# Optimization experiments

Measured on AMD Instinct MI355X. Metric: run time of the kernel, lower is better.

## Reference

```python
import jax, jax.numpy as jnp
import numpy as np

TAU = 0.07
EPS = 1e-6  # torch CosineSimilarity eps


def setup_inputs() -> dict:
    key = jax.random.key(0)
    k1, k2, k3 = jax.random.split(key, 3)
    n, d, n_classes = 8192, 256, 1024
    imitation_embeds = jax.random.normal(k1, (n, d), dtype=jnp.float32)
    recording_embeds = jax.random.normal(k2, (n, d), dtype=jnp.float32)
    labels = jax.random.randint(k3, (n,), 0, n_classes, dtype=jnp.int64)
    return {
        "imitation_embeds": imitation_embeds,
        "recording_embeds": recording_embeds,
        "labels": labels,
    }


def reference(imitation_embeds, recording_embeds, labels):
    n = imitation_embeds.shape[0]
    # cosine similarity with per-vector norm clamp (torch semantics)
    im_n = imitation_embeds / jnp.maximum(
        jnp.linalg.norm(imitation_embeds, axis=1, keepdims=True), EPS)
    rec_n = recording_embeds / jnp.maximum(
        jnp.linalg.norm(recording_embeds, axis=1, keepdims=True), EPS)
    i2r = jnp.einsum("nd,md->nm", im_n, rec_n) / TAU  # [n, n]

    same = labels[:, None] == labels[None, :]          # [n, n] bool
    eye = jnp.eye(n, dtype=bool)
    # original: mask = ~(same ^ diag_embed(diag(same))); diag(same) is all True
    # -> keep the diagonal (positive) and all different-label negatives
    mask = ~(same ^ eye)

    # per-row masked log-softmax evaluated at the diagonal entry:
    # log_softmax(row[mask])[pos_of_diag] = i2r[i,i] - logsumexp(row over mask)
    lse = jax.nn.logsumexp(jnp.where(mask, i2r, -jnp.inf), axis=1)  # [n]
    loss = -jnp.mean(jnp.diagonal(i2r) - lse)
    return loss
```

## Files before the change

kernel.cpp:

```cpp
#include <hip/hip_runtime.h>

#define N 8192
#define D 256
#define INV_TAU 14.285714285714286f
#define LOG2E 1.4426950408889634f
#define EPSN 1e-6f

#define RT 128
#define CT 64
#define CSPLIT 16
#define CPB (N / CSPLIT)
#define NTILES (CPB / CT)
#define MAXC 96

typedef unsigned int u32x4 __attribute__((ext_vector_type(4)));
typedef __bf16 bf16x8 __attribute__((ext_vector_type(8)));
typedef float f32x4 __attribute__((ext_vector_type(4)));

__device__ inline unsigned short f2bf(float x) {
    unsigned int u = __builtin_bit_cast(unsigned int, x);
    u += 0x7fffu + ((u >> 16) & 1u);
    return (unsigned short)(u >> 16);
}

__device__ inline float bf2f(unsigned short u) {
    return __builtin_bit_cast(float, (unsigned int)u << 16);
}

__global__ void ntx_prep(const float* __restrict__ im, const float* __restrict__ rec,
                         unsigned short* __restrict__ A, unsigned short* __restrict__ Bm,
                         float* __restrict__ diag, float* __restrict__ rowsum,
                         int* __restrict__ cnt, float* __restrict__ out) {
    const int wave = threadIdx.x >> 6;
    const int lane = threadIdx.x & 63;
    const int row  = blockIdx.x * 4 + wave;

    const float4 a = ((const float4*)(im  + (size_t)row * D))[lane];
    const float4 b = ((const float4*)(rec + (size_t)row * D))[lane];

    float ssa = a.x*a.x + a.y*a.y + a.z*a.z + a.w*a.w;
    float ssb = b.x*b.x + b.y*b.y + b.z*b.z + b.w*b.w;
    float dt  = a.x*b.x + a.y*b.y + a.z*b.z + a.w*b.w;
    #pragma unroll
    for (int o = 32; o; o >>= 1) {
        ssa += __shfl_xor(ssa, o);
        ssb += __shfl_xor(ssb, o);
        dt  += __shfl_xor(dt , o);
    }
    const float ra = 1.0f / fmaxf(sqrtf(ssa), EPSN);
    const float rb = 1.0f / fmaxf(sqrtf(ssb), EPSN);
    const float sa = ra * (INV_TAU * LOG2E);

    ushort4 pa, pb;
    pa.x = f2bf(a.x*sa); pa.y = f2bf(a.y*sa); pa.z = f2bf(a.z*sa); pa.w = f2bf(a.w*sa);
    pb.x = f2bf(b.x*rb); pb.y = f2bf(b.y*rb); pb.z = f2bf(b.z*rb); pb.w = f2bf(b.w*rb);
    *(ushort4*)(A  + (size_t)row * D + lane * 4) = pa;
    *(ushort4*)(Bm + (size_t)row * D + lane * 4) = pb;

    if (lane == 0) {
        diag[row]   = dt * ra * rb * INV_TAU;
        rowsum[row] = 0.0f;
    }
    if (blockIdx.x < 4) cnt[blockIdx.x * 256 + threadIdx.x] = 0;
    if (blockIdx.x == 0 && threadIdx.x == 0) out[0] = 0.0f;
}

__global__ void ntx_bucket(const int* __restrict__ labels, int* __restrict__ cnt,
                           int* __restrict__ bucket) {
    const int i = blockIdx.x * 256 + threadIdx.x;
    const int c = labels[i];
    const int pos = atomicAdd(&cnt[c], 1);
    if (pos < MAXC) bucket[c * MAXC + pos] = i;
}

__global__ void ntx_pairs(const unsigned short* __restrict__ A,
                          const unsigned short* __restrict__ Bm,
                          const int* __restrict__ labels,
                          const int* __restrict__ cnt, const int* __restrict__ bucket,
                          float* __restrict__ rowsum) {
    const int wave = threadIdx.x >> 6;
    const int lane = threadIdx.x & 63;
    const int i = blockIdx.x * 4 + wave;
    const int c = labels[i];
    const int m = min(cnt[c], MAXC);
    if (m < 2) return;

    const ushort4 av = *(const ushort4*)(A + (size_t)i * D + lane * 4);
    const float a0 = bf2f(av.x), a1 = bf2f(av.y), a2 = bf2f(av.z), a3 = bf2f(av.w);

    int jr_n = bucket[c * MAXC];
    ushort4 bv_n = *(const ushort4*)(Bm + (size_t)jr_n * D + lane * 4);

    float corr = 0.f;
    for (int j = 0; j < m; ++j) {
        const int jr = jr_n;
        const ushort4 bv = bv_n;
        if (j + 1 < m) {
            jr_n = bucket[c * MAXC + j + 1];
            bv_n = *(const ushort4*)(Bm + (size_t)jr_n * D + lane * 4);
        }
        if (jr == i) continue;
        float d = a0*bf2f(bv.x) + a1*bf2f(bv.y) + a2*bf2f(bv.z) + a3*bf2f(bv.w);
        #pragma unroll
        for (int o = 32; o; o >>= 1) d += __shfl_xor(d, o);
        corr += __builtin_amdgcn_exp2f(d);
    }
    if (lane == 0) atomicAdd(&rowsum[i], -corr);
}

__global__ __launch_bounds__(256, 3)
void ntx_lse(const unsigned short* __restrict__ A, const unsigned short* __restrict__ Bm,
             float* __restrict__ rowsum) {
    __shared__ __align__(128) unsigned char Bsb[CT * 512];

    const int wave = threadIdx.x >> 6;
    const int lane = threadIdx.x & 63;
    const int g    = lane >> 4;
    const int n16  = lane & 15;

    const int rowblk = blockIdx.x & (N / RT - 1);
    const int colblk = blockIdx.x >> 6;
    const int row0 = rowblk * RT + wave * 32;
    const int col0 = colblk * CPB;

    bf16x8 afrag[2][8];
    #pragma unroll
    for (int rs = 0; rs < 2; ++rs) {
        const int r = row0 + rs * 16 + n16;
        #pragma unroll
        for (int k = 0; k < 8; ++k)
            afrag[rs][k] = __builtin_bit_cast(
                bf16x8, *(const u32x4*)(A + (size_t)r * D + k * 32 + g * 8));
    }

    float acc[2][4] = {{0.f,0.f,0.f,0.f},{0.f,0.f,0.f,0.f}};

    const int c32 = threadIdx.x & 31;
    const int rr  = threadIdx.x >> 5;
    const int kk  = c32 >> 2;
    const int gg  = c32 & 3;
    const int xr  = (kk & 3) << 5;

    u32x4 stg[8];
    #pragma unroll
    for (int p = 0; p < 8; ++p)
        stg[p] = *(const u32x4*)(Bm + (size_t)(col0 + p * 8 + rr) * D + c32 * 8);

    for (int t = 0; t < NTILES; ++t) {
        #pragma unroll
        for (int p = 0; p < 8; ++p) {
            const int br = p * 8 + rr;
            const int off = (((((br >> 4) * 8 + kk) * 64) + gg * 16 + (br & 15)) * 16) ^ xr;
            *(u32x4*)(&Bsb[off]) = stg[p];
        }
        __syncthreads();

        if (t + 1 < NTILES) {
            const int coln = col0 + (t + 1) * CT;
            #pragma unroll
            for (int p = 0; p < 8; ++p)
                stg[p] = *(const u32x4*)(Bm + (size_t)(coln + p * 8 + rr) * D + c32 * 8);
        }

        #pragma unroll
        for (int cs = 0; cs < 4; ++cs) {
            bf16x8 bfrag[8];
            #pragma unroll
            for (int k = 0; k < 8; ++k)
                bfrag[k] = __builtin_bit_cast(
                    bf16x8, *(const u32x4*)(&Bsb[((((cs * 8 + k) * 64) + lane) * 16) ^ ((k & 3) << 5)]));

            #pragma unroll
            for (int rs = 0; rs < 2; ++rs) {
                f32x4 c = {0.f, 0.f, 0.f, 0.f};
                #pragma unroll
                for (int k = 0; k < 8; ++k)
                    c = __builtin_amdgcn_mfma_f32_16x16x32_bf16(
                            afrag[rs][k], bfrag[k], c, 0, 0, 0);
                #pragma unroll
                for (int q = 0; q < 4; ++q)
                    acc[rs][q] += __builtin_amdgcn_exp2f(c[q]);
            }
        }
        __syncthreads();
    }

    #pragma unroll
    for (int rs = 0; rs < 2; ++rs)
        #pragma unroll
        for (int q = 0; q < 4; ++q) {
            float v = acc[rs][q];
            v += __shfl_xor(v, 1);
            v += __shfl_xor(v, 2);
            v += __shfl_xor(v, 4);
            v += __shfl_xor(v, 8);
            if (n16 == 0)
                atomicAdd(&rowsum[row0 + rs * 16 + g * 4 + q], v);
        }
}

__global__ void ntx_finish(const float* __restrict__ diag,
                           const float* __restrict__ rowsum,
                           float* __restrict__ out) {
    __shared__ float red[4];
    const int i = blockIdx.x * 256 + threadIdx.x;
    float s = logf(rowsum[i]) - diag[i];
    #pragma unroll
    for (int o = 32; o; o >>= 1) s += __shfl_xor(s, o);
    if ((threadIdx.x & 63) == 0) red[threadIdx.x >> 6] = s;
    __syncthreads();
    if (threadIdx.x == 0)
        atomicAdd(out, (red[0] + red[1] + red[2] + red[3]) * (1.0f / (float)N));
}

extern "C" void kernel_launch(void* const* d_in, const int* in_sizes, int n_in,
                              void* d_out, int out_size, void* d_ws, size_t ws_size,
                              hipStream_t stream) {
    const float* im     = (const float*)d_in[0];
    const float* rec    = (const float*)d_in[1];
    const int*   labels = (const int*)d_in[2];
    float* out = (float*)d_out;

    unsigned short* A  = (unsigned short*)d_ws;
    unsigned short* Bm = A + (size_t)N * D;
    float* diag   = (float*)(Bm + (size_t)N * D);
    float* rowsum = diag + N;
    int*   cnt    = (int*)(rowsum + N);
    int*   bucket = cnt + 1024;

    ntx_prep<<<N / 4, 256, 0, stream>>>(im, rec, A, Bm, diag, rowsum, cnt, out);
    ntx_bucket<<<N / 256, 256, 0, stream>>>(labels, cnt, bucket);
    ntx_pairs<<<N / 4, 256, 0, stream>>>(A, Bm, labels, cnt, bucket, rowsum);
    ntx_lse<<<(N / RT) * CSPLIT, 256, 0, stream>>>(A, Bm, rowsum);
    ntx_finish<<<N / 256, 256, 0, stream>>>(diag, rowsum, out);
}
```

Before: 125.2 us.

## Double-buffer LSE tiles via direct global-to-LDS loads, grow row tile, fuse small kernels

The main LSE kernel now stages B tiles straight into double-buffered LDS with global_load_lds and uses one barrier per tile instead of a register staging pass with two syncs. The row tile doubles to 256, so each wave holds 64 rows of A fragments and the B tile is reused across more rows. Label bucketing moves into the prep kernel, and the same-label pair correction is merged with the final log and mean kernel, which cuts the launch count from five kernels to three plus a memset. In exchange, register pressure rises (occupancy hint drops to 2), the LDS swizzle is removed and may cause bank conflicts, and the grid has half as many blocks.

```diff
diff --git a/kernel.cpp b/kernel.cpp
--- a/kernel.cpp
+++ b/kernel.cpp
@@ -6,7 +6,7 @@
 #define LOG2E 1.4426950408889634f
 #define EPSN 1e-6f
 
-#define RT 128
+#define RT 256
 #define CT 64
 #define CSPLIT 16
 #define CPB (N / CSPLIT)
@@ -28,9 +28,11 @@
 }
 
 __global__ void ntx_prep(const float* __restrict__ im, const float* __restrict__ rec,
+                         const int* __restrict__ labels,
                          unsigned short* __restrict__ A, unsigned short* __restrict__ Bm,
                          float* __restrict__ diag, float* __restrict__ rowsum,
-                         int* __restrict__ cnt, float* __restrict__ out) {
+                         int* __restrict__ cnt, int* __restrict__ bucket,
+                         float* __restrict__ out) {
     const int wave = threadIdx.x >> 6;
     const int lane = threadIdx.x & 63;
     const int row  = blockIdx.x * 4 + wave;
@@ -60,58 +62,26 @@
     if (lane == 0) {
         diag[row]   = dt * ra * rb * INV_TAU;
         rowsum[row] = 0.0f;
-    }
-    if (blockIdx.x < 4) cnt[blockIdx.x * 256 + threadIdx.x] = 0;
+        const int c = labels[row];
+        const int pos = atomicAdd(&cnt[c], 1);
+        if (pos < MAXC) bucket[c * MAXC + pos] = row;
+    }
     if (blockIdx.x == 0 && threadIdx.x == 0) out[0] = 0.0f;
 }
 
-__global__ void ntx_bucket(const int* __restrict__ labels, int* __restrict__ cnt,
-                           int* __restrict__ bucket) {
-    const int i = blockIdx.x * 256 + threadIdx.x;
-    const int c = labels[i];
-    const int pos = atomicAdd(&cnt[c], 1);
-    if (pos < MAXC) bucket[c * MAXC + pos] = i;
-}
-
-__global__ void ntx_pairs(const unsigned short* __restrict__ A,
-                          const unsigned short* __restrict__ Bm,
-                          const int* __restrict__ labels,
-                          const int* __restrict__ cnt, const int* __restrict__ bucket,
-                          float* __restrict__ rowsum) {
-    const int wave = threadIdx.x >> 6;
-    const int lane = threadIdx.x & 63;
-    const int i = blockIdx.x * 4 + wave;
-    const int c = labels[i];
-    const int m = min(cnt[c], MAXC);
-    if (m < 2) return;
-
-    const ushort4 av = *(const ushort4*)(A + (size_t)i * D + lane * 4);
-    const float a0 = bf2f(av.x), a1 = bf2f(av.y), a2 = bf2f(av.z), a3 = bf2f(av.w);
-
-    int jr_n = bucket[c * MAXC];
-    ushort4 bv_n = *(const ushort4*)(Bm + (size_t)jr_n * D + lane * 4);
-
-    float corr = 0.f;
-    for (int j = 0; j < m; ++j) {
-        const int jr = jr_n;
-        const ushort4 bv = bv_n;
-        if (j + 1 < m) {
-            jr_n = bucket[c * MAXC + j + 1];
-            bv_n = *(const ushort4*)(Bm + (size_t)jr_n * D + lane * 4);
-        }
-        if (jr == i) continue;
-        float d = a0*bf2f(bv.x) + a1*bf2f(bv.y) + a2*bf2f(bv.z) + a3*bf2f(bv.w);
-        #pragma unroll
-        for (int o = 32; o; o >>= 1) d += __shfl_xor(d, o);
-        corr += __builtin_amdgcn_exp2f(d);
-    }
-    if (lane == 0) atomicAdd(&rowsum[i], -corr);
-}
-
-__global__ __launch_bounds__(256, 3)
+__device__ __forceinline__ void stage_tile(const unsigned short* gs, unsigned char* lb) {
+    #pragma unroll
+    for (int p = 0; p < 8; ++p)
+        __builtin_amdgcn_global_load_lds(
+            (const __attribute__((address_space(1))) unsigned int*)(gs + p * 32),
+            (__attribute__((address_space(3))) unsigned int*)(lb + p * 1024),
+            16, 0, 0);
+}
+
+__global__ __launch_bounds__(256, 2)
 void ntx_lse(const unsigned short* __restrict__ A, const unsigned short* __restrict__ Bm,
              float* __restrict__ rowsum) {
-    __shared__ __align__(128) unsigned char Bsb[CT * 512];
+    __shared__ __align__(128) unsigned char Bs[2][CT * 512];
 
     const int wave = threadIdx.x >> 6;
     const int lane = threadIdx.x & 63;
@@ -119,13 +89,13 @@
     const int n16  = lane & 15;
 
     const int rowblk = blockIdx.x & (N / RT - 1);
-    const int colblk = blockIdx.x >> 6;
-    const int row0 = rowblk * RT + wave * 32;
+    const int colblk = blockIdx.x >> 5;
+    const int row0 = rowblk * RT + wave * 64;
     const int col0 = colblk * CPB;
 
-    bf16x8 afrag[2][8];
-    #pragma unroll
-    for (int rs = 0; rs < 2; ++rs) {
+    bf16x8 afrag[4][8];
+    #pragma unroll
+    for (int rs = 0; rs < 4; ++rs) {
         const int r = row0 + rs * 16 + n16;
         #pragma unroll
         for (int k = 0; k < 8; ++k)
@@ -133,34 +103,25 @@
                 bf16x8, *(const u32x4*)(A + (size_t)r * D + k * 32 + g * 8));
     }
 
-    float acc[2][4] = {{0.f,0.f,0.f,0.f},{0.f,0.f,0.f,0.f}};
-
-    const int c32 = threadIdx.x & 31;
-    const int rr  = threadIdx.x >> 5;
-    const int kk  = c32 >> 2;
-    const int gg  = c32 & 3;
-    const int xr  = (kk & 3) << 5;
-
-    u32x4 stg[8];
-    #pragma unroll
-    for (int p = 0; p < 8; ++p)
-        stg[p] = *(const u32x4*)(Bm + (size_t)(col0 + p * 8 + rr) * D + c32 * 8);
+    float acc[4][4];
+    #pragma unroll
+    for (int rs = 0; rs < 4; ++rs)
+        #pragma unroll
+        for (int q = 0; q < 4; ++q) acc[rs][q] = 0.f;
+
+    const unsigned short* gsrc0 = Bm + (size_t)(col0 + wave * 16 + n16) * D + g * 8;
+    unsigned char* lds0 = &Bs[0][wave * 8192];
+    unsigned char* lds1 = &Bs[1][wave * 8192];
+
+    stage_tile(gsrc0, lds0);
+    asm volatile("s_waitcnt vmcnt(0)" ::: "memory");
+    __builtin_amdgcn_s_barrier();
+    __builtin_amdgcn_sched_barrier(0);
 
     for (int t = 0; t < NTILES; ++t) {
-        #pragma unroll
-        for (int p = 0; p < 8; ++p) {
-            const int br = p * 8 + rr;
-            const int off = (((((br >> 4) * 8 + kk) * 64) + gg * 16 + (br & 15)) * 16) ^ xr;
-            *(u32x4*)(&Bsb[off]) = stg[p];
-        }
-        __syncthreads();
-
-        if (t + 1 < NTILES) {
-            const int coln = col0 + (t + 1) * CT;
-            #pragma unroll
-            for (int p = 0; p < 8; ++p)
-                stg[p] = *(const u32x4*)(Bm + (size_t)(coln + p * 8 + rr) * D + c32 * 8);
-        }
+        const int buf = t & 1;
+        if (t + 1 < NTILES)
+            stage_tile(gsrc0 + (size_t)(t + 1) * CT * D, buf ? lds0 : lds1);
 
         #pragma unroll
         for (int cs = 0; cs < 4; ++cs) {
@@ -168,10 +129,10 @@
             #pragma unroll
             for (int k = 0; k < 8; ++k)
                 bfrag[k] = __builtin_bit_cast(
-                    bf16x8, *(const u32x4*)(&Bsb[((((cs * 8 + k) * 64) + lane) * 16) ^ ((k & 3) << 5)]));
+                    bf16x8, *(const u32x4*)(&Bs[buf][(cs * 8 + k) * 1024 + lane * 16]));
 
             #pragma unroll
-            for (int rs = 0; rs < 2; ++rs) {
+            for (int rs = 0; rs < 4; ++rs) {
                 f32x4 c = {0.f, 0.f, 0.f, 0.f};
                 #pragma unroll
                 for (int k = 0; k < 8; ++k)
@@ -182,11 +143,14 @@
                     acc[rs][q] += __builtin_amdgcn_exp2f(c[q]);
             }
         }
-        __syncthreads();
-    }
-
-    #pragma unroll
-    for (int rs = 0; rs < 2; ++rs)
+
+        asm volatile("s_waitcnt vmcnt(0)" ::: "memory");
+        __builtin_amdgcn_s_barrier();
+        __builtin_amdgcn_sched_barrier(0);
+    }
+
+    #pragma unroll
+    for (int rs = 0; rs < 4; ++rs)
         #pragma unroll
         for (int q = 0; q < 4; ++q) {
             float v = acc[rs][q];
@@ -199,15 +163,42 @@
         }
 }
 
-__global__ void ntx_finish(const float* __restrict__ diag,
-                           const float* __restrict__ rowsum,
-                           float* __restrict__ out) {
+__global__ void ntx_pfin(const unsigned short* __restrict__ A,
+                         const unsigned short* __restrict__ Bm,
+                         const int* __restrict__ labels,
+                         const int* __restrict__ cnt, const int* __restrict__ bucket,
+                         const float* __restrict__ diag, const float* __restrict__ rowsum,
+                         float* __restrict__ out) {
     __shared__ float red[4];
-    const int i = blockIdx.x * 256 + threadIdx.x;
-    float s = logf(rowsum[i]) - diag[i];
-    #pragma unroll
-    for (int o = 32; o; o >>= 1) s += __shfl_xor(s, o);
-    if ((threadIdx.x & 63) == 0) red[threadIdx.x >> 6] = s;
+    const int wave = threadIdx.x >> 6;
+    const int lane = threadIdx.x & 63;
+    const int i = blockIdx.x * 4 + wave;
+    const int c = labels[i];
+    const int m = min(cnt[c], MAXC);
+
+    float corr = 0.f;
+    if (m >= 2) {
+        const ushort4 av = *(const ushort4*)(A + (size_t)i * D + lane * 4);
+        const float a0 = bf2f(av.x), a1 = bf2f(av.y), a2 = bf2f(av.z), a3 = bf2f(av.w);
+
+        int jr_n = bucket[c * MAXC];
+        ushort4 bv_n = *(const ushort4*)(Bm + (size_t)jr_n * D + lane * 4);
+
+        for (int j = 0; j < m; ++j) {
+            const int jr = jr_n;
+            const ushort4 bv = bv_n;
+            if (j + 1 < m) {
+                jr_n = bucket[c * MAXC + j + 1];
+                bv_n = *(const ushort4*)(Bm + (size_t)jr_n * D + lane * 4);
+            }
+            if (jr == i) continue;
+            float d = a0*bf2f(bv.x) + a1*bf2f(bv.y) + a2*bf2f(bv.z) + a3*bf2f(bv.w);
+            #pragma unroll
+            for (int o = 32; o; o >>= 1) d += __shfl_xor(d, o);
+            corr += __builtin_amdgcn_exp2f(d);
+        }
+    }
+    if (lane == 0) red[wave] = logf(rowsum[i] - corr) - diag[i];
     __syncthreads();
     if (threadIdx.x == 0)
         atomicAdd(out, (red[0] + red[1] + red[2] + red[3]) * (1.0f / (float)N));
@@ -228,9 +219,8 @@
     int*   cnt    = (int*)(rowsum + N);
     int*   bucket = cnt + 1024;
 
-    ntx_prep<<<N / 4, 256, 0, stream>>>(im, rec, A, Bm, diag, rowsum, cnt, out);
-    ntx_bucket<<<N / 256, 256, 0, stream>>>(labels, cnt, bucket);
-    ntx_pairs<<<N / 4, 256, 0, stream>>>(A, Bm, labels, cnt, bucket, rowsum);
+    hipMemsetAsync(cnt, 0, 1024 * sizeof(int), stream);
+    ntx_prep<<<N / 4, 256, 0, stream>>>(im, rec, labels, A, Bm, diag, rowsum, cnt, bucket, out);
     ntx_lse<<<(N / RT) * CSPLIT, 256, 0, stream>>>(A, Bm, rowsum);
-    ntx_finish<<<N / 256, 256, 0, stream>>>(diag, rowsum, out);
-}
+    ntx_pfin<<<N / 4, 256, 0, stream>>>(A, Bm, labels, cnt, bucket, diag, rowsum, out);
+}
```

Result: slower. 141.0 us (+12.7%).
